# Kernel optimization log

Hardware: AMD Instinct MI355X
Metric: run time of the kernel (lower is better)

Reference implementation:

```python
import jax, jax.numpy as jnp
import numpy as np

N_NODES = 100000


def _sage_conv(x, src, dst, W_l, b_l, W_r):
    # PyG SAGEConv (aggr='mean', root_weight=True):
    #   out = lin_l(mean_{j in N(i)} x_j) + lin_r(x_i)
    agg = jax.ops.segment_sum(x[src], dst, num_segments=N_NODES)          # [N, d]
    cnt = jax.ops.segment_sum(jnp.ones(src.shape[0], x.dtype), dst,
                              num_segments=N_NODES)                        # [N]
    mean = agg / jnp.maximum(cnt, 1.0)[:, None]                            # isolated nodes -> 0
    return mean @ W_l + b_l + x @ W_r


def setup_inputs() -> dict:
    key = jax.random.key(0)
    ks = jax.random.split(key, 8)
    dim_in, dim_h, dim_out = 128, 256, 64
    n_edges = 1600000
    x = jax.random.normal(ks[0], (N_NODES, dim_in), dtype=jnp.float32)
    edge_index = jax.random.randint(ks[1], (2, n_edges), 0, N_NODES, dtype=jnp.int32)
    s1 = 1.0 / np.sqrt(dim_in)
    s2 = 1.0 / np.sqrt(dim_h)
    return {
        "x": x,
        "edge_index": edge_index,
        "W1_l": jax.random.uniform(ks[2], (dim_in, dim_h), jnp.float32, -s1, s1),
        "b1": jnp.zeros((dim_h,), jnp.float32),
        "W1_r": jax.random.uniform(ks[3], (dim_in, dim_h), jnp.float32, -s1, s1),
        "W2_l": jax.random.uniform(ks[4], (dim_h, dim_out), jnp.float32, -s2, s2),
        "b2": jnp.zeros((dim_out,), jnp.float32),
        "W2_r": jax.random.uniform(ks[5], (dim_h, dim_out), jnp.float32, -s2, s2),
    }


def reference(x, edge_index, W1_l, b1, W1_r, W2_l, b2, W2_r):
    src, dst = edge_index[0], edge_index[1]
    h = _sage_conv(x, src, dst, W1_l, b1, W1_r)
    h = jax.nn.relu(h)
    # dropout p=0.5 is identity in eval mode (deterministic reference)
    h = _sage_conv(h, src, dst, W2_l, b2, W2_r)
    return jax.nn.log_softmax(h, axis=1)
```

## Files before the change

kernel.cpp:

```cpp
#include <hip/hip_runtime.h>

#define N_NODES 100000
#define N_EDGES 1600000
#define GK 256
#define NBKT 196
#define NBIN 128
#define EPB (N_EDGES / NBIN)

typedef __attribute__((ext_vector_type(8))) short bf16x8;
typedef __attribute__((ext_vector_type(4))) float f32x4;
typedef __attribute__((ext_vector_type(2))) float f32x2;
typedef unsigned short ushort_t;

__device__ __forceinline__ float bf2f(unsigned int bits16) {
  union { unsigned int i; float f; } v; v.i = bits16 << 16; return v.f;
}
__device__ __forceinline__ unsigned short f2bf(float f) {
  union { float f; unsigned int i; } v; v.f = f;
  unsigned int u = v.i;
  unsigned int r = (u + 0x7fffu + ((u >> 16) & 1u)) >> 16;
  return (unsigned short)r;
}
__device__ __forceinline__ unsigned pkbf(f32x2 a) {
  return (unsigned)f2bf(a[0]) | ((unsigned)f2bf(a[1]) << 16);
}
__device__ __forceinline__ void gload16(const void* g, void* l) {
  __builtin_amdgcn_global_load_lds(
      (const __attribute__((address_space(1))) void*)g,
      (__attribute__((address_space(3))) void*)l, 16, 0, 0);
}

#define ACC_U32(u, b) \
  acc[b] += __builtin_amdgcn_cvt_pk_f32_fp8((u), false); \
  acc[(b) + 1] += __builtin_amdgcn_cvt_pk_f32_fp8((u), true);
#define ACC_U4(U, b) \
  ACC_U32((U).x, (b)) ACC_U32((U).y, (b) + 2) ACC_U32((U).z, (b) + 4) ACC_U32((U).w, (b) + 6)

#define CVT_X_WORK (N_NODES * 32)
#define CVT_TOTAL (CVT_X_WORK + 65536 + 32768)
__global__ void count_cvt_kernel(const int* __restrict__ dst, int* __restrict__ partialHist,
                                 const float* __restrict__ x,
                                 const float* __restrict__ W1l, const float* __restrict__ W1r,
                                 const float* __restrict__ W2l, const float* __restrict__ W2r,
                                 ushort_t* __restrict__ axb, unsigned int* __restrict__ xq,
                                 ushort_t* __restrict__ W1bt, ushort_t* __restrict__ W2bt) {
  __shared__ int hist[NBKT];
  int tid = threadIdx.x;
  if (blockIdx.x < NBIN) {
    for (int i = tid; i < NBKT; i += 256) hist[i] = 0;
    __syncthreads();
    const int4* d4 = (const int4*)(dst + blockIdx.x * EPB);
    for (int i = tid; i < EPB / 4; i += 256) {
      int4 v = d4[i];
      atomicAdd(&hist[v.x >> 9], 1); atomicAdd(&hist[v.y >> 9], 1);
      atomicAdd(&hist[v.z >> 9], 1); atomicAdd(&hist[v.w >> 9], 1);
    }
    __syncthreads();
    for (int i = tid; i < NBKT; i += 256) partialHist[i * NBIN + blockIdx.x] = hist[i];
  } else {
    int idx = (blockIdx.x - NBIN) * 256 + tid;
    if (idx < CVT_X_WORK) {
      int n = idx >> 5, j = (idx & 31) << 2;
      float4 v = *(const float4*)(x + (size_t)n * 128 + j);
      ushort4 o;
      o.x = f2bf(v.x); o.y = f2bf(v.y); o.z = f2bf(v.z); o.w = f2bf(v.w);
      *(ushort4*)(axb + (size_t)n * 256 + 128 + j) = o;
      unsigned int q = __builtin_amdgcn_cvt_pk_fp8_f32(v.x, v.y, 0, false);
      q = __builtin_amdgcn_cvt_pk_fp8_f32(v.z, v.w, q, true);
      xq[(size_t)n * 32 + (j >> 2)] = q;
    } else if (idx < CVT_X_WORK + 65536) {
      int t = idx - CVT_X_WORK;
      int n = t >> 8, k = t & 255;
      float v = (k < 128) ? W1l[(size_t)k * 256 + n] : W1r[(size_t)(k - 128) * 256 + n];
      W1bt[t] = f2bf(v);
    } else if (idx < CVT_TOTAL) {
      int t = idx - CVT_X_WORK - 65536;
      int n = t >> 8, k = t & 255;
      float v = (n < 64) ? W2l[(size_t)k * 64 + n] : W2r[(size_t)k * 64 + (n - 64)];
      W2bt[t] = f2bf(v);
    }
  }
}

__global__ void scan_buckets_kernel(const int* __restrict__ ph, int* __restrict__ base,
                                    int* __restrict__ cursor, int* __restrict__ rowptr) {
  __shared__ int wsum[4];
  int t = threadIdx.x;
  int v = 0;
  if (t < NBKT) {
    const int* row = ph + t * NBIN;
    for (int b = 0; b < NBIN; ++b) v += row[b];
  }
  int lane = t & 63, wave = t >> 6;
  int s = v;
#pragma unroll
  for (int o = 1; o < 64; o <<= 1) { int u = __shfl_up(s, o); if (lane >= o) s += u; }
  if (lane == 63) wsum[wave] = s;
  __syncthreads();
  if (t == 0) { int c = 0; for (int k = 0; k < 4; ++k) { int u = wsum[k]; wsum[k] = c; c += u; } }
  __syncthreads();
  int excl = s - v + wsum[wave];
  if (t < NBKT) { base[t] = excl; cursor[t] = excl; }
  if (t == 0) { base[NBKT] = N_EDGES; rowptr[N_NODES] = N_EDGES; }
}

__global__ void bin_scatter_kernel(const int* __restrict__ src, const int* __restrict__ dst,
                                   int* __restrict__ cursor, unsigned int* __restrict__ pairs) {
  __shared__ int hist[NBKT];
  __shared__ int curs[NBKT];
  int tid = threadIdx.x;
  for (int i = tid; i < NBKT; i += 256) hist[i] = 0;
  __syncthreads();
  const int4* d4 = (const int4*)(dst + blockIdx.x * EPB);
  const int4* s4 = (const int4*)(src + blockIdx.x * EPB);
  for (int i = tid; i < EPB / 4; i += 256) {
    int4 v = d4[i];
    atomicAdd(&hist[v.x >> 9], 1); atomicAdd(&hist[v.y >> 9], 1);
    atomicAdd(&hist[v.z >> 9], 1); atomicAdd(&hist[v.w >> 9], 1);
  }
  __syncthreads();
  for (int i = tid; i < NBKT; i += 256) curs[i] = atomicAdd(&cursor[i], hist[i]);
  __syncthreads();
  for (int i = tid; i < EPB / 4; i += 256) {
    int4 v = d4[i];
    int4 u = s4[i];
    int p;
    p = atomicAdd(&curs[v.x >> 9], 1); pairs[p] = ((unsigned)(v.x & 511) << 17) | (unsigned)u.x;
    p = atomicAdd(&curs[v.y >> 9], 1); pairs[p] = ((unsigned)(v.y & 511) << 17) | (unsigned)u.y;
    p = atomicAdd(&curs[v.z >> 9], 1); pairs[p] = ((unsigned)(v.z & 511) << 17) | (unsigned)u.z;
    p = atomicAdd(&curs[v.w >> 9], 1); pairs[p] = ((unsigned)(v.w & 511) << 17) | (unsigned)u.w;
  }
}

__launch_bounds__(256)
__global__ void bucket_csr_kernel(const unsigned int* __restrict__ pairs,
                                  const int* __restrict__ base,
                                  int* __restrict__ rowptr, int* __restrict__ ebuf) {
  __shared__ int hist[512];
  __shared__ int curs[512];
  __shared__ int wsum[4];
  int b = blockIdx.x;
  int tid = threadIdx.x;
  int n0 = b << 9;
  int nn = N_NODES - n0; if (nn > 512) nn = 512;
  int lo = base[b], hi = base[b + 1];
  hist[tid] = 0; hist[tid + 256] = 0;
  __syncthreads();
  for (int i = lo + tid; i < hi; i += 256)
    atomicAdd(&hist[pairs[i] >> 17], 1);
  __syncthreads();
  int h0 = hist[2 * tid], h1 = hist[2 * tid + 1];
  int ps = h0 + h1;
  int lane = tid & 63, wave = tid >> 6;
  int s = ps;
#pragma unroll
  for (int o = 1; o < 64; o <<= 1) { int t = __shfl_up(s, o); if (lane >= o) s += t; }
  if (lane == 63) wsum[wave] = s;
  __syncthreads();
  if (tid == 0) { int c = 0; for (int k = 0; k < 4; ++k) { int t = wsum[k]; wsum[k] = c; c += t; } }
  __syncthreads();
  int base0 = lo + (s - ps) + wsum[wave];
  curs[2 * tid] = base0;
  curs[2 * tid + 1] = base0 + h0;
  if (2 * tid < nn)     rowptr[n0 + 2 * tid] = base0;
  if (2 * tid + 1 < nn) rowptr[n0 + 2 * tid + 1] = base0 + h0;
  __syncthreads();
  for (int i = lo + tid; i < hi; i += 256) {
    unsigned int p = pairs[i];
    int pos = atomicAdd(&curs[p >> 17], 1);
    ebuf[pos] = (int)(p & 0x1FFFF);
  }
}

__launch_bounds__(256)
__global__ void agg_mean1_kernel(const int* __restrict__ rowptr, const int* __restrict__ ebuf,
                                 const uint4* __restrict__ xq4, ushort_t* __restrict__ axb) {
  int t = blockIdx.x * 256 + threadIdx.x;
  int node = t >> 3, q = t & 7;
  bool valid = node < N_NODES;
  int anode = valid ? node : 0;
  int beg = rowptr[anode], end = rowptr[anode + 1];
  if (!valid) end = beg;
  f32x2 acc[8];
#pragma unroll
  for (int i = 0; i < 8; ++i) acc[i] = (f32x2){0.f, 0.f};
  int e = beg;
  for (; e + 8 <= end; e += 8) {
    int s0 = ebuf[e], s1 = ebuf[e + 1], s2 = ebuf[e + 2], s3 = ebuf[e + 3];
    int s4 = ebuf[e + 4], s5 = ebuf[e + 5], s6 = ebuf[e + 6], s7 = ebuf[e + 7];
    uint4 a = xq4[(unsigned)(s0 * 8 + q)];
    uint4 b = xq4[(unsigned)(s1 * 8 + q)];
    uint4 c = xq4[(unsigned)(s2 * 8 + q)];
    uint4 d = xq4[(unsigned)(s3 * 8 + q)];
    uint4 f = xq4[(unsigned)(s4 * 8 + q)];
    uint4 g = xq4[(unsigned)(s5 * 8 + q)];
    uint4 h2 = xq4[(unsigned)(s6 * 8 + q)];
    uint4 k = xq4[(unsigned)(s7 * 8 + q)];
    ACC_U4(a, 0) ACC_U4(b, 0) ACC_U4(c, 0) ACC_U4(d, 0)
    ACC_U4(f, 0) ACC_U4(g, 0) ACC_U4(h2, 0) ACC_U4(k, 0)
  }
  for (; e < end; ++e) {
    int s = ebuf[e];
    uint4 a = xq4[(unsigned)(s * 8 + q)];
    ACC_U4(a, 0)
  }
  if (!valid) return;
  float inv = (end > beg) ? 1.0f / (float)(end - beg) : 0.0f;
  f32x2 inv2 = {inv, inv};
#pragma unroll
  for (int i = 0; i < 8; ++i) acc[i] *= inv2;
  uint4* orow = (uint4*)(axb + (size_t)node * 256 + q * 16);
  uint4 o0, o1;
  o0.x = pkbf(acc[0]); o0.y = pkbf(acc[1]); o0.z = pkbf(acc[2]); o0.w = pkbf(acc[3]);
  o1.x = pkbf(acc[4]); o1.y = pkbf(acc[5]); o1.z = pkbf(acc[6]); o1.w = pkbf(acc[7]);
  orow[0] = o0;
  orow[1] = o1;
}

template<int MODE>
__launch_bounds__(256)
__global__ void gemm_bf16_kernel(const ushort_t* __restrict__ A, const ushort_t* __restrict__ Bt,
                                 const float* __restrict__ bias, ushort_t* __restrict__ C,
                                 unsigned char* __restrict__ P8, ushort_t* __restrict__ QB,
                                 int M, int NC) {
  __shared__ ushort_t ldsA[128 * 64];
  __shared__ ushort_t ldsB[128 * 64];
  const int tid = threadIdx.x;
  const int lane = tid & 63;
  const int wm = (tid >> 6) & 1, wn = tid >> 7;
  const int rowBase = blockIdx.x * 128;
  const int colBase = blockIdx.y * 128;
  f32x4 acc[4][4];
#pragma unroll
  for (int i = 0; i < 4; ++i)
#pragma unroll
    for (int j = 0; j < 4; ++j) acc[i][j] = (f32x4){0.f, 0.f, 0.f, 0.f};

  for (int k0 = 0; k0 < GK; k0 += 64) {
#pragma unroll
    for (int i = 0; i < 4; ++i) {
      int s = tid + i * 256;
      int row = s >> 3, off16 = s & 7;
      int k16 = off16 ^ (row & 7);
      int ga = rowBase + row; if (ga > M - 1) ga = M - 1;
      gload16(A + (size_t)ga * GK + k0 + k16 * 8, &ldsA[s * 8]);
      gload16(Bt + (size_t)(colBase + row) * GK + k0 + k16 * 8, &ldsB[s * 8]);
    }
    __syncthreads();
#pragma unroll
    for (int kc = 0; kc < 2; ++kc) {
      bf16x8 af[4], bfr[4];
#pragma unroll
      for (int i = 0; i < 4; ++i) {
        int rA = wm * 64 + i * 16 + (lane & 15);
        int oA = (kc * 4 + (lane >> 4)) ^ (rA & 7);
        af[i] = *(const bf16x8*)&ldsA[rA * 64 + oA * 8];
        int rB = wn * 64 + i * 16 + (lane & 15);
        int oB = (kc * 4 + (lane >> 4)) ^ (rB & 7);
        bfr[i] = *(const bf16x8*)&ldsB[rB * 64 + oB * 8];
      }
#pragma unroll
      for (int mi = 0; mi < 4; ++mi)
#pragma unroll
        for (int ni = 0; ni < 4; ++ni)
          acc[mi][ni] = __builtin_amdgcn_mfma_f32_16x16x32_bf16(af[mi], bfr[ni], acc[mi][ni], 0, 0, 0);
    }
    __syncthreads();
  }
#pragma unroll
  for (int mi = 0; mi < 4; ++mi) {
#pragma unroll
    for (int r = 0; r < 4; ++r) {
      int grow = rowBase + wm * 64 + mi * 16 + (lane >> 4) * 4 + r;
      if (grow >= M) continue;
#pragma unroll
      for (int ni = 0; ni < 4; ++ni) {
        float v = acc[mi][ni][r];
        if (MODE == 0) {
          int gcol = colBase + wn * 64 + ni * 16 + (lane & 15);
          C[(size_t)grow * NC + gcol] = f2bf(fmaxf(v + bias[gcol], 0.f));
        } else {
          int c = ni * 16 + (lane & 15);
          if (wn == 0) {
            unsigned int u = __builtin_amdgcn_cvt_pk_fp8_f32(v, v, 0, false);
            P8[(size_t)grow * 64 + c] = (unsigned char)(u & 0xff);
          } else {
            QB[(size_t)grow * 64 + c] = f2bf(v);
          }
        }
      }
    }
  }
}

__launch_bounds__(256)
__global__ void final_kernel(const int* __restrict__ rowptr, const int* __restrict__ ebuf,
                             const uint4* __restrict__ p84, const ushort_t* __restrict__ qb,
                             const float* __restrict__ b2, float* __restrict__ out) {
  int t = blockIdx.x * 256 + threadIdx.x;
  int node = t >> 2, q = t & 3;
  bool valid = node < N_NODES;
  int anode = valid ? node : 0;
  int beg = rowptr[anode], end = rowptr[anode + 1];
  if (!valid) end = beg;
  f32x2 acc[8];
#pragma unroll
  for (int i = 0; i < 8; ++i) acc[i] = (f32x2){0.f, 0.f};
  int e = beg;
  for (; e + 4 <= end; e += 4) {
    int s0 = ebuf[e], s1 = ebuf[e + 1], s2 = ebuf[e + 2], s3 = ebuf[e + 3];
    uint4 a = p84[(unsigned)(s0 * 4 + q)];
    uint4 b = p84[(unsigned)(s1 * 4 + q)];
    uint4 c = p84[(unsigned)(s2 * 4 + q)];
    uint4 d = p84[(unsigned)(s3 * 4 + q)];
    ACC_U4(a, 0) ACC_U4(b, 0) ACC_U4(c, 0) ACC_U4(d, 0)
  }
  for (; e < end; ++e) {
    int s = ebuf[e];
    uint4 a = p84[(unsigned)(s * 4 + q)];
    ACC_U4(a, 0)
  }
  float inv = (end > beg) ? 1.0f / (float)(end - beg) : 0.0f;
  f32x2 inv2 = {inv, inv};
#pragma unroll
  for (int i = 0; i < 8; ++i) acc[i] *= inv2;
  const uint4* qrow = (const uint4*)(qb + (size_t)anode * 64 + q * 16);
  const float* bb = b2 + q * 16;
#pragma unroll
  for (int k = 0; k < 2; ++k) {
    uint4 qv = qrow[k];
    acc[4 * k + 0][0] += bb[8 * k + 0] + bf2f(qv.x & 0xffff);
    acc[4 * k + 0][1] += bb[8 * k + 1] + bf2f(qv.x >> 16);
    acc[4 * k + 1][0] += bb[8 * k + 2] + bf2f(qv.y & 0xffff);
    acc[4 * k + 1][1] += bb[8 * k + 3] + bf2f(qv.y >> 16);
    acc[4 * k + 2][0] += bb[8 * k + 4] + bf2f(qv.z & 0xffff);
    acc[4 * k + 2][1] += bb[8 * k + 5] + bf2f(qv.z >> 16);
    acc[4 * k + 3][0] += bb[8 * k + 6] + bf2f(qv.w & 0xffff);
    acc[4 * k + 3][1] += bb[8 * k + 7] + bf2f(qv.w >> 16);
  }
  float mx[8];
#pragma unroll
  for (int i = 0; i < 8; ++i) mx[i] = fmaxf(acc[i][0], acc[i][1]);
#pragma unroll
  for (int s = 4; s >= 1; s >>= 1)
#pragma unroll
    for (int j = 0; j < 4; ++j)
      if (j < s) mx[j] = fmaxf(mx[j], mx[j + s]);
  float m = mx[0];
  m = fmaxf(m, __shfl_xor(m, 1));
  m = fmaxf(m, __shfl_xor(m, 2));
  float sm[8];
#pragma unroll
  for (int i = 0; i < 8; ++i)
    sm[i] = __expf(acc[i][0] - m) + __expf(acc[i][1] - m);
#pragma unroll
  for (int s = 4; s >= 1; s >>= 1)
#pragma unroll
    for (int j = 0; j < 4; ++j)
      if (j < s) sm[j] += sm[j + s];
  float ssum = sm[0];
  ssum += __shfl_xor(ssum, 1);
  ssum += __shfl_xor(ssum, 2);
  if (!valid) return;
  float ls = m + __logf(ssum);
  f32x2 ls2 = {ls, ls};
  float4* orow = (float4*)(out + (size_t)node * 64 + q * 16);
#pragma unroll
  for (int i = 0; i < 4; ++i) {
    f32x2 a = acc[2 * i] - ls2;
    f32x2 b = acc[2 * i + 1] - ls2;
    float4 o = {a[0], a[1], b[0], b[1]};
    orow[i] = o;
  }
}


extern "C" void kernel_launch(void* const* d_in, const int* in_sizes, int n_in,
                              void* d_out, int out_size, void* d_ws, size_t ws_size,
                              hipStream_t stream) {
  const float* x   = (const float*)d_in[0];
  const int*   ei  = (const int*)d_in[1];
  const float* W1l = (const float*)d_in[2];
  const float* b1  = (const float*)d_in[3];
  const float* W1r = (const float*)d_in[4];
  const float* W2l = (const float*)d_in[5];
  const float* b2  = (const float*)d_in[6];
  const float* W2r = (const float*)d_in[7];
  float* out = (float*)d_out;
  const int* src = ei;
  const int* dst = ei + N_EDGES;

  char* w = (char*)d_ws;
  int*      bucketBase  = (int*)(w);
  int*      bucketCur   = (int*)(w + 1024);
  int*      partialHist = (int*)(w + 2048);
  int*      rowptr      = (int*)(w + 128ull * 1024);
  int*      ebuf        = (int*)(w + 1024ull * 1024);
  ushort_t* W1bt        = (ushort_t*)(w + 8ull * 1024 * 1024);
  ushort_t* W2bt        = (ushort_t*)(w + 8ull * 1024 * 1024 + 256 * 1024);
  ushort_t* axb         = (ushort_t*)(w + 9ull * 1024 * 1024);
  ushort_t* h           = (ushort_t*)(w + 61ull * 1024 * 1024);
  unsigned int* pairs   = (unsigned int*)(w + 61ull * 1024 * 1024);
  unsigned int* xq      = (unsigned int*)(w + 113ull * 1024 * 1024);
  unsigned int* p8      = (unsigned int*)(w + 126ull * 1024 * 1024);
  ushort_t*     qb      = (ushort_t*)(w + 133ull * 1024 * 1024);

  const int CVT_BLOCKS = (CVT_TOTAL + 255) / 256;
  count_cvt_kernel<<<NBIN + CVT_BLOCKS, 256, 0, stream>>>(
      dst, partialHist, x, W1l, W1r, W2l, W2r, axb, xq, W1bt, W2bt);
  scan_buckets_kernel<<<1, 256, 0, stream>>>(partialHist, bucketBase, bucketCur, rowptr);
  bin_scatter_kernel<<<NBIN, 256, 0, stream>>>(src, dst, bucketCur, pairs);
  bucket_csr_kernel<<<NBKT, 256, 0, stream>>>(pairs, bucketBase, rowptr, ebuf);

  agg_mean1_kernel<<<(8 * N_NODES + 255) / 256, 256, 0, stream>>>(
      rowptr, ebuf, (const uint4*)xq, axb);

  gemm_bf16_kernel<0><<<dim3((N_NODES + 127) / 128, 2), 256, 0, stream>>>(
      axb, W1bt, b1, h, nullptr, nullptr, N_NODES, 256);
  gemm_bf16_kernel<1><<<dim3((N_NODES + 127) / 128, 1), 256, 0, stream>>>(
      h, W2bt, nullptr, nullptr, (unsigned char*)p8, qb, N_NODES, 128);

  final_kernel<<<(4 * N_NODES + 255) / 256, 256, 0, stream>>>(
      rowptr, ebuf, (const uint4*)p8, qb, b2, out);
}
```

Baseline: 186.9 us.

## Fuse both layer GEMMs keeping hidden tile in LDS; halve per-thread agg width

The two back-to-back GEMMs are merged into one kernel. Each 128-row block computes the ReLU hidden activations in two 128-column halves, stores each half as swizzled bf16 in LDS, and immediately multiplies it by the matching slice of W2. This removes the global write and re-read of the full hidden matrix and one kernel launch, at the cost of 64KB of LDS per block and lower occupancy. Separately, the first aggregation kernel now uses 16 threads per node with 8-byte gathers instead of 8 threads with 16-byte gathers, trading more threads for fewer registers per thread.

```diff
diff --git a/kernel.cpp b/kernel.cpp
--- a/kernel.cpp
+++ b/kernel.cpp
@@ -174,98 +174,150 @@
 
 __launch_bounds__(256)
 __global__ void agg_mean1_kernel(const int* __restrict__ rowptr, const int* __restrict__ ebuf,
-                                 const uint4* __restrict__ xq4, ushort_t* __restrict__ axb) {
+                                 const uint2* __restrict__ xq2, ushort_t* __restrict__ axb) {
   int t = blockIdx.x * 256 + threadIdx.x;
-  int node = t >> 3, q = t & 7;
+  int node = t >> 4, q = t & 15;
   bool valid = node < N_NODES;
   int anode = valid ? node : 0;
   int beg = rowptr[anode], end = rowptr[anode + 1];
   if (!valid) end = beg;
-  f32x2 acc[8];
-#pragma unroll
-  for (int i = 0; i < 8; ++i) acc[i] = (f32x2){0.f, 0.f};
+  f32x2 acc[4];
+#pragma unroll
+  for (int i = 0; i < 4; ++i) acc[i] = (f32x2){0.f, 0.f};
   int e = beg;
-  for (; e + 8 <= end; e += 8) {
+  for (; e + 4 <= end; e += 4) {
     int s0 = ebuf[e], s1 = ebuf[e + 1], s2 = ebuf[e + 2], s3 = ebuf[e + 3];
-    int s4 = ebuf[e + 4], s5 = ebuf[e + 5], s6 = ebuf[e + 6], s7 = ebuf[e + 7];
-    uint4 a = xq4[(unsigned)(s0 * 8 + q)];
-    uint4 b = xq4[(unsigned)(s1 * 8 + q)];
-    uint4 c = xq4[(unsigned)(s2 * 8 + q)];
-    uint4 d = xq4[(unsigned)(s3 * 8 + q)];
-    uint4 f = xq4[(unsigned)(s4 * 8 + q)];
-    uint4 g = xq4[(unsigned)(s5 * 8 + q)];
-    uint4 h2 = xq4[(unsigned)(s6 * 8 + q)];
-    uint4 k = xq4[(unsigned)(s7 * 8 + q)];
-    ACC_U4(a, 0) ACC_U4(b, 0) ACC_U4(c, 0) ACC_U4(d, 0)
-    ACC_U4(f, 0) ACC_U4(g, 0) ACC_U4(h2, 0) ACC_U4(k, 0)
+    uint2 a = xq2[(unsigned)(s0 * 16 + q)];
+    uint2 b = xq2[(unsigned)(s1 * 16 + q)];
+    uint2 c = xq2[(unsigned)(s2 * 16 + q)];
+    uint2 d = xq2[(unsigned)(s3 * 16 + q)];
+    ACC_U32(a.x, 0) ACC_U32(a.y, 2)
+    ACC_U32(b.x, 0) ACC_U32(b.y, 2)
+    ACC_U32(c.x, 0) ACC_U32(c.y, 2)
+    ACC_U32(d.x, 0) ACC_U32(d.y, 2)
   }
   for (; e < end; ++e) {
     int s = ebuf[e];
-    uint4 a = xq4[(unsigned)(s * 8 + q)];
-    ACC_U4(a, 0)
+    uint2 a = xq2[(unsigned)(s * 16 + q)];
+    ACC_U32(a.x, 0) ACC_U32(a.y, 2)
   }
   if (!valid) return;
   float inv = (end > beg) ? 1.0f / (float)(end - beg) : 0.0f;
   f32x2 inv2 = {inv, inv};
 #pragma unroll
-  for (int i = 0; i < 8; ++i) acc[i] *= inv2;
-  uint4* orow = (uint4*)(axb + (size_t)node * 256 + q * 16);
-  uint4 o0, o1;
-  o0.x = pkbf(acc[0]); o0.y = pkbf(acc[1]); o0.z = pkbf(acc[2]); o0.w = pkbf(acc[3]);
-  o1.x = pkbf(acc[4]); o1.y = pkbf(acc[5]); o1.z = pkbf(acc[6]); o1.w = pkbf(acc[7]);
-  orow[0] = o0;
-  orow[1] = o1;
-}
-
-template<int MODE>
+  for (int i = 0; i < 4; ++i) acc[i] *= inv2;
+  uint2 o;
+  o.x = pkbf(acc[0]);
+  o.y = pkbf(acc[1]);
+  uint2 o2;
+  o2.x = pkbf(acc[2]);
+  o2.y = pkbf(acc[3]);
+  uint4 ov = {o.x, o.y, o2.x, o2.y};
+  *(uint4*)(axb + (size_t)node * 256 + q * 8) = ov;
+}
+
 __launch_bounds__(256)
-__global__ void gemm_bf16_kernel(const ushort_t* __restrict__ A, const ushort_t* __restrict__ Bt,
-                                 const float* __restrict__ bias, ushort_t* __restrict__ C,
-                                 unsigned char* __restrict__ P8, ushort_t* __restrict__ QB,
-                                 int M, int NC) {
+__global__ void gemm_fused_kernel(const ushort_t* __restrict__ A,
+                                  const ushort_t* __restrict__ W1bt,
+                                  const ushort_t* __restrict__ W2bt,
+                                  const float* __restrict__ b1,
+                                  unsigned char* __restrict__ P8, ushort_t* __restrict__ QB,
+                                  int M) {
   __shared__ ushort_t ldsA[128 * 64];
   __shared__ ushort_t ldsB[128 * 64];
+  __shared__ ushort_t ldsH[128 * 128];
   const int tid = threadIdx.x;
   const int lane = tid & 63;
   const int wm = (tid >> 6) & 1, wn = tid >> 7;
   const int rowBase = blockIdx.x * 128;
-  const int colBase = blockIdx.y * 128;
-  f32x4 acc[4][4];
+  f32x4 acc2[4][4];
 #pragma unroll
   for (int i = 0; i < 4; ++i)
 #pragma unroll
-    for (int j = 0; j < 4; ++j) acc[i][j] = (f32x4){0.f, 0.f, 0.f, 0.f};
-
-  for (int k0 = 0; k0 < GK; k0 += 64) {
-#pragma unroll
-    for (int i = 0; i < 4; ++i) {
-      int s = tid + i * 256;
-      int row = s >> 3, off16 = s & 7;
-      int k16 = off16 ^ (row & 7);
-      int ga = rowBase + row; if (ga > M - 1) ga = M - 1;
-      gload16(A + (size_t)ga * GK + k0 + k16 * 8, &ldsA[s * 8]);
-      gload16(Bt + (size_t)(colBase + row) * GK + k0 + k16 * 8, &ldsB[s * 8]);
+    for (int j = 0; j < 4; ++j) acc2[i][j] = (f32x4){0.f, 0.f, 0.f, 0.f};
+
+  for (int hp = 0; hp < 2; ++hp) {
+    f32x4 acc1[4][4];
+#pragma unroll
+    for (int i = 0; i < 4; ++i)
+#pragma unroll
+      for (int j = 0; j < 4; ++j) acc1[i][j] = (f32x4){0.f, 0.f, 0.f, 0.f};
+    for (int k0 = 0; k0 < 256; k0 += 64) {
+#pragma unroll
+      for (int i = 0; i < 4; ++i) {
+        int s = tid + i * 256;
+        int row = s >> 3, off16 = s & 7;
+        int k16 = off16 ^ (row & 7);
+        int ga = rowBase + row; if (ga > M - 1) ga = M - 1;
+        gload16(A + (size_t)ga * 256 + k0 + k16 * 8, &ldsA[s * 8]);
+        gload16(W1bt + (size_t)(hp * 128 + row) * 256 + k0 + k16 * 8, &ldsB[s * 8]);
+      }
+      __syncthreads();
+#pragma unroll
+      for (int kc = 0; kc < 2; ++kc) {
+        bf16x8 af[4], bg[4];
+#pragma unroll
+        for (int i = 0; i < 4; ++i) {
+          int rA = wm * 64 + i * 16 + (lane & 15);
+          int oA = (kc * 4 + (lane >> 4)) ^ (rA & 7);
+          af[i] = *(const bf16x8*)&ldsA[rA * 64 + oA * 8];
+          int rB = wn * 64 + i * 16 + (lane & 15);
+          int oB = (kc * 4 + (lane >> 4)) ^ (rB & 7);
+          bg[i] = *(const bf16x8*)&ldsB[rB * 64 + oB * 8];
+        }
+#pragma unroll
+        for (int mi = 0; mi < 4; ++mi)
+#pragma unroll
+          for (int ni = 0; ni < 4; ++ni)
+            acc1[mi][ni] = __builtin_amdgcn_mfma_f32_16x16x32_bf16(af[mi], bg[ni], acc1[mi][ni], 0, 0, 0);
+      }
+      __syncthreads();
+    }
+#pragma unroll
+    for (int mi = 0; mi < 4; ++mi) {
+#pragma unroll
+      for (int r = 0; r < 4; ++r) {
+        int row = wm * 64 + mi * 16 + (lane >> 4) * 4 + r;
+#pragma unroll
+        for (int ni = 0; ni < 4; ++ni) {
+          int colh = wn * 64 + ni * 16 + (lane & 15);
+          float v = fmaxf(acc1[mi][ni][r] + b1[hp * 128 + colh], 0.f);
+          int ss = (colh >> 3) ^ (row & 15);
+          ldsH[row * 128 + ss * 8 + (colh & 7)] = f2bf(v);
+        }
+      }
     }
     __syncthreads();
-#pragma unroll
-    for (int kc = 0; kc < 2; ++kc) {
-      bf16x8 af[4], bfr[4];
+    for (int kk = 0; kk < 128; kk += 64) {
 #pragma unroll
       for (int i = 0; i < 4; ++i) {
-        int rA = wm * 64 + i * 16 + (lane & 15);
-        int oA = (kc * 4 + (lane >> 4)) ^ (rA & 7);
-        af[i] = *(const bf16x8*)&ldsA[rA * 64 + oA * 8];
-        int rB = wn * 64 + i * 16 + (lane & 15);
-        int oB = (kc * 4 + (lane >> 4)) ^ (rB & 7);
-        bfr[i] = *(const bf16x8*)&ldsB[rB * 64 + oB * 8];
-      }
-#pragma unroll
-      for (int mi = 0; mi < 4; ++mi)
-#pragma unroll
-        for (int ni = 0; ni < 4; ++ni)
-          acc[mi][ni] = __builtin_amdgcn_mfma_f32_16x16x32_bf16(af[mi], bfr[ni], acc[mi][ni], 0, 0, 0);
-    }
-    __syncthreads();
+        int s = tid + i * 256;
+        int row = s >> 3, off16 = s & 7;
+        int k16 = off16 ^ (row & 7);
+        gload16(W2bt + (size_t)row * 256 + hp * 128 + kk + k16 * 8, &ldsB[s * 8]);
+      }
+      __syncthreads();
+#pragma unroll
+      for (int kc = 0; kc < 2; ++kc) {
+        bf16x8 af[4], bg[4];
+#pragma unroll
+        for (int i = 0; i < 4; ++i) {
+          int rA = wm * 64 + i * 16 + (lane & 15);
+          int slot = (kk >> 3) + kc * 4 + (lane >> 4);
+          int ss = slot ^ (rA & 15);
+          af[i] = *(const bf16x8*)&ldsH[rA * 128 + ss * 8];
+          int rB = wn * 64 + i * 16 + (lane & 15);
+          int oB = (kc * 4 + (lane >> 4)) ^ (rB & 7);
+          bg[i] = *(const bf16x8*)&ldsB[rB * 64 + oB * 8];
+        }
+#pragma unroll
+        for (int mi = 0; mi < 4; ++mi)
+#pragma unroll
+          for (int ni = 0; ni < 4; ++ni)
+            acc2[mi][ni] = __builtin_amdgcn_mfma_f32_16x16x32_bf16(af[mi], bg[ni], acc2[mi][ni], 0, 0, 0);
+      }
+      __syncthreads();
+    }
   }
 #pragma unroll
   for (int mi = 0; mi < 4; ++mi) {
@@ -275,18 +327,13 @@
       if (grow >= M) continue;
 #pragma unroll
       for (int ni = 0; ni < 4; ++ni) {
-        float v = acc[mi][ni][r];
-        if (MODE == 0) {
-          int gcol = colBase + wn * 64 + ni * 16 + (lane & 15);
-          C[(size_t)grow * NC + gcol] = f2bf(fmaxf(v + bias[gcol], 0.f));
+        float v = acc2[mi][ni][r];
+        int c = ni * 16 + (lane & 15);
+        if (wn == 0) {
+          unsigned int u = __builtin_amdgcn_cvt_pk_fp8_f32(v, v, 0, false);
+          P8[(size_t)grow * 64 + c] = (unsigned char)(u & 0xff);
         } else {
-          int c = ni * 16 + (lane & 15);
-          if (wn == 0) {
-            unsigned int u = __builtin_amdgcn_cvt_pk_fp8_f32(v, v, 0, false);
-            P8[(size_t)grow * 64 + c] = (unsigned char)(u & 0xff);
-          } else {
-            QB[(size_t)grow * 64 + c] = f2bf(v);
-          }
+          QB[(size_t)grow * 64 + c] = f2bf(v);
         }
       }
     }
@@ -399,7 +446,6 @@
   ushort_t* W1bt        = (ushort_t*)(w + 8ull * 1024 * 1024);
   ushort_t* W2bt        = (ushort_t*)(w + 8ull * 1024 * 1024 + 256 * 1024);
   ushort_t* axb         = (ushort_t*)(w + 9ull * 1024 * 1024);
-  ushort_t* h           = (ushort_t*)(w + 61ull * 1024 * 1024);
   unsigned int* pairs   = (unsigned int*)(w + 61ull * 1024 * 1024);
   unsigned int* xq      = (unsigned int*)(w + 113ull * 1024 * 1024);
   unsigned int* p8      = (unsigned int*)(w + 126ull * 1024 * 1024);
@@ -412,13 +458,11 @@
   bin_scatter_kernel<<<NBIN, 256, 0, stream>>>(src, dst, bucketCur, pairs);
   bucket_csr_kernel<<<NBKT, 256, 0, stream>>>(pairs, bucketBase, rowptr, ebuf);
 
-  agg_mean1_kernel<<<(8 * N_NODES + 255) / 256, 256, 0, stream>>>(
-      rowptr, ebuf, (const uint4*)xq, axb);
-
-  gemm_bf16_kernel<0><<<dim3((N_NODES + 127) / 128, 2), 256, 0, stream>>>(
-      axb, W1bt, b1, h, nullptr, nullptr, N_NODES, 256);
-  gemm_bf16_kernel<1><<<dim3((N_NODES + 127) / 128, 1), 256, 0, stream>>>(
-      h, W2bt, nullptr, nullptr, (unsigned char*)p8, qb, N_NODES, 128);
+  agg_mean1_kernel<<<(16 * N_NODES + 255) / 256, 256, 0, stream>>>(
+      rowptr, ebuf, (const uint2*)xq, axb);
+
+  gemm_fused_kernel<<<(N_NODES + 127) / 128, 256, 0, stream>>>(
+      axb, W1bt, W2bt, b1, (unsigned char*)p8, qb, N_NODES);
 
   final_kernel<<<(4 * N_NODES + 255) / 256, 256, 0, stream>>>(
       rowptr, ebuf, (const uint4*)p8, qb, b2, out);
```

Measured after the change: 203.4 us. 1.09x slower.
